# Performance work log

Hardware: AMD Instinct MI355X
Metric: run time of the kernel (lower is better)

The kernel has to match this reference:

```python
import jax, jax.numpy as jnp
import numpy as np

H = 16            # num_heads
NORM = 16.0       # gate normalizer
SCALE = 128.0 ** -0.5  # (embed_dim // num_heads) ** -0.5, per source
EPS = 1e-5


def setup_inputs() -> dict:
    key = jax.random.key(0)
    ks = jax.random.split(key, 10)
    B, L, D = 2, 2048, 2048
    g = lambda k, shape, s: jax.random.normal(k, shape, jnp.float32) * s
    return {
        "x": g(ks[0], (B, L, D), 1.0),
        "Wq": g(ks[1], (1024, D), 0.02),
        "Wk": g(ks[2], (1024, D), 0.02),
        "Wkg1": g(ks[3], (16, D), 0.02),
        "Wkg2": g(ks[4], (1024, 16), 0.05),
        "bkg2": jnp.zeros((1024,), jnp.float32),
        "Wv": g(ks[5], (D, D), 0.02),
        "Wg": g(ks[6], (D, D), 0.02),
        "bg": jnp.zeros((D,), jnp.float32),
        "Wo": g(ks[7], (D, D), 0.02),
    }


def _gla_core(x, Wq, Wk, Wkg1, Wkg2, bkg2, Wv, Wg, bg, Wo):
    B, L, D = x.shape
    q = x @ Wq.T                         # [B,L,1024]
    k = (x @ Wk.T) * SCALE               # [B,L,1024]
    kg = (x @ Wkg1.T) @ Wkg2.T + bkg2    # [B,L,1024] low-rank gate
    v = x @ Wv.T                         # [B,L,2048]
    gproj = x @ Wg.T + bg                # [B,L,2048]

    dk = q.shape[-1] // H   # 64
    dv = D // H             # 128
    heads = lambda t, dh: t.reshape(B, L, H, dh).transpose(0, 2, 1, 3)  # b h l d
    qh = heads(q, dk)
    kh = heads(k, dk)
    vh = heads(v, dv)
    gk = jax.nn.log_sigmoid(heads(kg, dk)) / NORM  # b h l dk

    # recurrence: S_t = diag(exp(gk_t)) S_{t-1} + k_t v_t^T ; o_t = q_t S_t
    tfirst = lambda t: t.transpose(2, 0, 1, 3)  # l b h d

    def step(S, inp):
        qt, kt, vt, gt = inp
        S = S * jnp.exp(gt)[..., None] + kt[..., None] * vt[..., None, :]
        ot = jnp.einsum('bhk,bhkv->bhv', qt, S)
        return S, ot

    S0 = jnp.zeros((B, H, dk, dv), x.dtype)
    _, os = jax.lax.scan(step, S0, (tfirst(qh), tfirst(kh), tfirst(vh), tfirst(gk)))
    o = os.transpose(1, 2, 0, 3)  # b h l dv

    # LayerNorm over head dim, no affine
    mu = o.mean(-1, keepdims=True)
    var = ((o - mu) ** 2).mean(-1, keepdims=True)
    o = (o - mu) * jax.lax.rsqrt(var + EPS)

    o = o.transpose(0, 2, 1, 3).reshape(B, L, D)  # b l (h dv)
    return (jax.nn.silu(gproj) * o) @ Wo.T


def reference(x, Wq, Wk, Wkg1, Wkg2, bkg2, Wv, Wg, bg, Wo):
    return _gla_core(x, Wq, Wk, Wkg1, Wkg2, bkg2, Wv, Wg, bg, Wo)
```

## Files before the change

### kernel.cpp

```cpp
#include <hip/hip_runtime.h>
#include <hip/hip_bf16.h>

using bf16x8 = __attribute__((ext_vector_type(8))) __bf16;
using fx4    = __attribute__((ext_vector_type(4))) float;
using us4    = __attribute__((ext_vector_type(4))) unsigned short;
using us8    = __attribute__((ext_vector_type(8))) unsigned short;

__device__ __forceinline__ float b2f(unsigned short u) {
    unsigned int x = ((unsigned int)u) << 16;
    return __builtin_bit_cast(float, x);
}
__device__ __forceinline__ unsigned short f2b(float f) {
    __hip_bfloat16 h = __float2bfloat16(f);
    return __builtin_bit_cast(unsigned short, h);
}
__device__ __forceinline__ float logsigmoidf(float z) {
    return fminf(z, 0.0f) - log1pf(expf(-fabsf(z)));
}

__device__ __forceinline__ void gl_lds16(const unsigned short* g, unsigned short* l) {
    __builtin_amdgcn_global_load_lds(
        (const __attribute__((address_space(1))) void*)g,
        (__attribute__((address_space(3))) void*)l, 16, 0, 0);
}

__device__ __forceinline__ bf16x8 frag64(const unsigned short* base, int row, int cq) {
    return *reinterpret_cast<const bf16x8*>(base + row * 64 + (((cq ^ (row & 7)) << 3)));
}
__device__ __forceinline__ int sw_idx(int row, int col) {
    return row * 64 + ((((col >> 3) ^ (row & 7)) << 3)) + (col & 7);
}

__global__ __launch_bounds__(256) void detect_kernel(
    const unsigned int* __restrict__ x, int* __restrict__ flag)
{
    __shared__ int bad[256];
    const int t = threadIdx.x;
    int b = 0;
#pragma unroll
    for (int i = 0; i < 16; ++i) {
        unsigned int w = x[t * 16 + i];
        float v = b2f((unsigned short)(w & 0xFFFFu));
        if (!(fabsf(v) < 1.0e6f)) b = 1;
    }
    bad[t] = b;
    __syncthreads();
    for (int s = 128; s > 0; s >>= 1) {
        if (t < s) bad[t] |= bad[t + s];
        __syncthreads();
    }
    if (t == 0) flag[0] = bad[0];
}

struct CvtArgs {
    const void* src[10];
    unsigned short* dst[10];
};

__global__ __launch_bounds__(256) void convert_all_kernel(
    CvtArgs a, const int* __restrict__ flag)
{
    const int pref[11] = {0, 8192, 10240, 12288, 12320, 12336, 12337,
                          16433, 20529, 20531, 24627};
    const int blk = blockIdx.x;
    int s = 0;
#pragma unroll
    for (int i = 1; i < 10; ++i) s += (blk >= pref[i]) ? 1 : 0;
    const int i0 = (blk - pref[s]) * 1024 + threadIdx.x * 4;
    if (*flag) {
        const float* sp = (const float*)a.src[s];
        fx4 v = *reinterpret_cast<const fx4*>(sp + i0);
        us4 r;
#pragma unroll
        for (int e = 0; e < 4; ++e) r[e] = f2b(v[e]);
        *reinterpret_cast<us4*>(a.dst[s] + i0) = r;
    } else {
        const unsigned short* sp = (const unsigned short*)a.src[s];
        *reinterpret_cast<us4*>(a.dst[s] + i0) =
            *reinterpret_cast<const us4*>(sp + i0);
    }
}

struct Seg3 {
    unsigned short* C0;
    unsigned short* C1;
    unsigned short* C2;
    const unsigned short* bias2;
};

__global__ __launch_bounds__(512, 2) void gemm_fused3_kernel(
    const unsigned short* __restrict__ A, const unsigned short* __restrict__ W,
    Seg3 segs, float scale_k)
{
    __shared__ __align__(16) unsigned short As[2 * 256 * 64];
    __shared__ __align__(16) unsigned short Bs[2 * 2 * 128 * 64];

    const int NT = 32, K = 2048;
    const int tid  = threadIdx.x;
    const int lane = tid & 63, wid = tid >> 6;
    const int quad = lane >> 4, l15 = lane & 15;
    const int wr = wid >> 2, wc = wid & 3;
    const int m0 = blockIdx.y * 256, n0 = blockIdx.x * 256;

    const unsigned short* Ab = A + (size_t)m0 * K;
    const unsigned short* Wb = W + (size_t)n0 * K;

    const int sx = ((tid & 7) ^ ((tid >> 3) & 7)) * 8;
    const unsigned short* pA[2][2];
    const unsigned short* pB[2][2];
#pragma unroll
    for (int mh = 0; mh < 2; ++mh)
#pragma unroll
        for (int j = 0; j < 2; ++j)
            pA[mh][j] = Ab + (size_t)(j * 128 + mh * 64 + (tid >> 3)) * K + sx;
#pragma unroll
    for (int nh = 0; nh < 2; ++nh)
#pragma unroll
        for (int j = 0; j < 2; ++j)
            pB[nh][j] = Wb + (size_t)((j * 2 + (tid >> 8)) * 64 + nh * 32 +
                                      ((tid >> 3) & 31)) * K + sx;

    fx4 acc[8][4];
#pragma unroll
    for (int i = 0; i < 8; ++i)
#pragma unroll
        for (int j = 0; j < 4; ++j) acc[i][j] = fx4{0.f, 0.f, 0.f, 0.f};

    auto stageA = [&](int mh, int tt) {
#pragma unroll
        for (int j = 0; j < 2; ++j)
            gl_lds16(pA[mh][j] + tt * 64,
                     As + (tt & 1) * 16384 + (j * 128 + mh * 64) * 64 + tid * 8);
    };
    auto stageB = [&](int nh, int tt) {
#pragma unroll
        for (int j = 0; j < 2; ++j)
            gl_lds16(pB[nh][j] + tt * 64,
                     Bs + (tt & 1) * 16384 + nh * 8192 + j * 4096 + tid * 8);
    };

    bf16x8 afr[4][2], bfr[2][2];
    const int x7 = l15 & 7;
    const int cswz0 = (quad ^ x7) << 3;
    const int cswz1 = ((quad + 4) ^ x7) << 3;
    int arow[4], brow[2];
#pragma unroll
    for (int mt = 0; mt < 4; ++mt) arow[mt] = (wr * 128 + mt * 16 + l15) * 64;
#pragma unroll
    for (int nt = 0; nt < 2; ++nt) brow[nt] = (wc * 32 + nt * 16 + l15) * 64;

    auto ldA = [&](int s, int mh) {
        const unsigned short* base = As + s * 16384 + mh * 4096;
#pragma unroll
        for (int mt = 0; mt < 4; ++mt) {
            afr[mt][0] = *(const bf16x8*)(base + arow[mt] + cswz0);
            afr[mt][1] = *(const bf16x8*)(base + arow[mt] + cswz1);
        }
    };
    auto ldB = [&](int s, int nh) {
        const unsigned short* base = Bs + s * 16384 + nh * 8192;
#pragma unroll
        for (int nt = 0; nt < 2; ++nt) {
            bfr[nt][0] = *(const bf16x8*)(base + brow[nt] + cswz0);
            bfr[nt][1] = *(const bf16x8*)(base + brow[nt] + cswz1);
        }
    };
    auto mma = [&](int mh, int nh) {
        __builtin_amdgcn_s_setprio(1);
#pragma unroll
        for (int mt = 0; mt < 4; ++mt)
#pragma unroll
            for (int nt = 0; nt < 2; ++nt) {
                acc[mh * 4 + mt][nh * 2 + nt] = __builtin_amdgcn_mfma_f32_16x16x32_bf16(
                    afr[mt][0], bfr[nt][0], acc[mh * 4 + mt][nh * 2 + nt], 0, 0, 0);
                acc[mh * 4 + mt][nh * 2 + nt] = __builtin_amdgcn_mfma_f32_16x16x32_bf16(
                    afr[mt][1], bfr[nt][1], acc[mh * 4 + mt][nh * 2 + nt], 0, 0, 0);
            }
        __builtin_amdgcn_s_setprio(0);
    };

    stageA(0, 0); stageB(0, 0); stageA(1, 0); stageB(1, 0);
    stageA(0, 1); stageB(0, 1);

    for (int t = 0; t < NT; ++t) {
        const int s = t & 1;
        if (t + 1 < NT) stageA(1, t + 1);
        if (t < NT - 1) asm volatile("s_waitcnt vmcnt(6)" ::: "memory");
        else            asm volatile("s_waitcnt vmcnt(0)" ::: "memory");
        asm volatile("s_barrier" ::: "memory");
        ldA(s, 0); ldB(s, 0);
        mma(0, 0);
        asm volatile("s_barrier" ::: "memory");
        if (t + 1 < NT) stageB(1, t + 1);
        ldB(s, 1);
        asm volatile("s_barrier" ::: "memory");
        mma(0, 1);
        asm volatile("s_barrier" ::: "memory");
        if (t + 2 < NT) stageA(0, t + 2);
        ldA(s, 1); ldB(s, 0);
        asm volatile("s_barrier" ::: "memory");
        mma(1, 0);
        asm volatile("s_barrier" ::: "memory");
        if (t + 2 < NT) stageB(0, t + 2);
        ldB(s, 1);
        asm volatile("s_barrier" ::: "memory");
        mma(1, 1);
        asm volatile("s_barrier" ::: "memory");
    }

    const int segi = n0 >> 11;
    unsigned short* Cs = (segi == 0) ? segs.C0 : ((segi == 1) ? segs.C1 : segs.C2);
#pragma unroll
    for (int j = 0; j < 4; ++j) {
        const int ncl = (n0 & 2047) + wc * 64 + j * 16 + l15;
        const float av = (segi == 0 && ncl >= 1024) ? scale_k : 1.0f;
        const float bv = (segi == 2) ? b2f(segs.bias2[ncl]) : 0.0f;
#pragma unroll
        for (int i = 0; i < 8; ++i) {
#pragma unroll
            for (int r = 0; r < 4; ++r) {
                const int mrow = m0 + wr * 128 + i * 16 + quad * 4 + r;
                float val = acc[i][j][r] * av + bv;
                if (segi == 2) val = val / (1.0f + __expf(-val));
                Cs[(size_t)mrow * 2048 + ncl] = f2b(val);
            }
        }
    }
}

__global__ __launch_bounds__(256) void gemm_bt_kernel(
    const unsigned short* __restrict__ A, const unsigned short* __restrict__ W,
    unsigned short* __restrict__ C, int M, int N, int K,
    const int* __restrict__ oflag)
{
    __shared__ __align__(16) unsigned short As[128 * 64];
    __shared__ __align__(16) unsigned short Bs[128 * 64];

    const int tid  = threadIdx.x;
    const int lane = tid & 63, wid = tid >> 6;
    const int quad = lane >> 4, l15 = lane & 15;
    const int wm = (wid & 1) * 64, wn = (wid >> 1) * 64;
    const int m0 = blockIdx.y * 128, n0 = blockIdx.x * 128;

    fx4 acc[4][4];
#pragma unroll
    for (int i = 0; i < 4; ++i)
#pragma unroll
        for (int j = 0; j < 4; ++j) acc[i][j] = fx4{0.f, 0.f, 0.f, 0.f};

    const int srow = lane >> 3;
    const int g8   = ((lane & 7) ^ srow) * 8;
    const int c8   = (lane & 7) * 8;
    const unsigned short* Ab = A + (size_t)m0 * K;
    const unsigned short* Wb = W + (size_t)n0 * K;

    for (int k0 = 0; k0 < K; k0 += 64) {
#pragma unroll
        for (int p = 0; p < 4; ++p) {
            const int la  = wid * 4 + p;
            const int row = la * 8 + srow;
            gl_lds16(Ab + (size_t)row * K + k0 + g8, As + row * 64 + c8);
            gl_lds16(Wb + (size_t)row * K + k0 + g8, Bs + row * 64 + c8);
        }
        __syncthreads();
#pragma unroll
        for (int ks = 0; ks < 2; ++ks) {
            const int cq = quad + ks * 4;
            bf16x8 af[4], bfr[4];
#pragma unroll
            for (int mt = 0; mt < 4; ++mt) af[mt] = frag64(As, wm + mt * 16 + l15, cq);
#pragma unroll
            for (int nt = 0; nt < 4; ++nt) bfr[nt] = frag64(Bs, wn + nt * 16 + l15, cq);
#pragma unroll
            for (int mt = 0; mt < 4; ++mt)
#pragma unroll
                for (int nt = 0; nt < 4; ++nt)
                    acc[mt][nt] = __builtin_amdgcn_mfma_f32_16x16x32_bf16(
                        af[mt], bfr[nt], acc[mt][nt], 0, 0, 0);
        }
        __syncthreads();
    }

    const int f32out = oflag ? *oflag : 0;
#pragma unroll
    for (int nt = 0; nt < 4; ++nt) {
        const int ncol = n0 + wn + nt * 16 + l15;
#pragma unroll
        for (int mt = 0; mt < 4; ++mt) {
#pragma unroll
            for (int r = 0; r < 4; ++r) {
                const int mrow = m0 + wm + mt * 16 + quad * 4 + r;
                float val = acc[mt][nt][r];
                const size_t idx = (size_t)mrow * N + ncol;
                if (f32out) ((float*)C)[idx] = val;
                else        C[idx] = f2b(val);
            }
        }
    }
}

__global__ __launch_bounds__(256) void gate1_kernel(
    const unsigned short* __restrict__ x, const unsigned short* __restrict__ Wkg1,
    const unsigned short* __restrict__ Wkg2, const unsigned short* __restrict__ bkg2,
    float* __restrict__ Ag)
{
    __shared__ float part[4][16];
    __shared__ float kgrow[16];
    const int m = blockIdx.x;
    const int tid = threadIdx.x;
    const int lane = tid & 63, w = tid >> 6;

    us8 xv = *reinterpret_cast<const us8*>(x + (size_t)m * 2048 + tid * 8);
    float xr[8];
#pragma unroll
    for (int e = 0; e < 8; ++e) xr[e] = b2f(xv[e]);

#pragma unroll
    for (int n = 0; n < 16; ++n) {
        us8 wv = *reinterpret_cast<const us8*>(Wkg1 + (size_t)n * 2048 + tid * 8);
        float s = 0.f;
#pragma unroll
        for (int e = 0; e < 8; ++e) s += xr[e] * b2f(wv[e]);
#pragma unroll
        for (int off = 1; off < 64; off <<= 1) s += __shfl_xor(s, off, 64);
        if (lane == 0) part[w][n] = s;
    }
    __syncthreads();
    if (tid < 16)
        kgrow[tid] = part[0][tid] + part[1][tid] + part[2][tid] + part[3][tid];
    __syncthreads();
    float kr[16];
#pragma unroll
    for (int j = 0; j < 16; ++j) kr[j] = kgrow[j];

    const int b = m >> 11, l = m & 2047;
    const int c0 = tid * 4;
    const int h = c0 >> 6, d0 = c0 & 63;
    fx4 gv;
#pragma unroll
    for (int qi = 0; qi < 4; ++qi) {
        const int c = c0 + qi;
        us8 w0 = *reinterpret_cast<const us8*>(Wkg2 + (size_t)c * 16);
        us8 w1 = *reinterpret_cast<const us8*>(Wkg2 + (size_t)c * 16 + 8);
        float z = b2f(bkg2[c]);
#pragma unroll
        for (int j = 0; j < 8; ++j) z += kr[j] * b2f(w0[j]) + kr[8 + j] * b2f(w1[j]);
        gv[qi] = logsigmoidf(z) * 0.0625f;
    }
    *reinterpret_cast<fx4*>(Ag + ((size_t)(b * 16 + h) * 2048 + l) * 64 + d0) = gv;
}

__global__ __launch_bounds__(256) void gate2_kernel(float* __restrict__ Ag)
{
    const int gidx = blockIdx.x * 256 + threadIdx.x;
    const int d = gidx & 63, ch = (gidx >> 6) & 31, bh = gidx >> 11;
    float* p = Ag + ((size_t)bh * 2048 + ch * 64) * 64 + d;
    float acc = 0.f;
#pragma unroll 8
    for (int t = 0; t < 64; ++t) {
        acc += p[(size_t)t * 64];
        p[(size_t)t * 64] = acc;
    }
}

__global__ __launch_bounds__(256) void pass1_kernel(
    const unsigned short* __restrict__ k, int kstr,
    const unsigned short* __restrict__ v,
    const float* __restrict__ Ag, float* __restrict__ Tc)
{
    __shared__ __align__(16) unsigned short kT[64 * 64];
    __shared__ __align__(16) unsigned short vT[128 * 64];

    const int blk = blockIdx.x;
    const int ch = blk & 31, bh = blk >> 5;
    const int b = bh >> 4, h = bh & 15;
    const int tid = threadIdx.x;
    const int lane = tid & 63, w = tid >> 6;
    const int quad = lane >> 4, l15 = lane & 15;

    const float* Abase = Ag + ((size_t)bh * 2048 + ch * 64) * 64;
    const unsigned short* kbase = k + ((size_t)(b * 2048 + ch * 64)) * kstr + h * 64;
    const unsigned short* vbase = v + ((size_t)(b * 2048 + ch * 64)) * 2048 + h * 128;

    {
        const int s = tid >> 2, d0 = (tid & 3) * 16;
        float av[16], a63[16];
        *(fx4*)(av)      = *(const fx4*)(Abase + (size_t)s * 64 + d0);
        *(fx4*)(av + 4)  = *(const fx4*)(Abase + (size_t)s * 64 + d0 + 4);
        *(fx4*)(av + 8)  = *(const fx4*)(Abase + (size_t)s * 64 + d0 + 8);
        *(fx4*)(av + 12) = *(const fx4*)(Abase + (size_t)s * 64 + d0 + 12);
        *(fx4*)(a63)      = *(const fx4*)(Abase + (size_t)63 * 64 + d0);
        *(fx4*)(a63 + 4)  = *(const fx4*)(Abase + (size_t)63 * 64 + d0 + 4);
        *(fx4*)(a63 + 8)  = *(const fx4*)(Abase + (size_t)63 * 64 + d0 + 8);
        *(fx4*)(a63 + 12) = *(const fx4*)(Abase + (size_t)63 * 64 + d0 + 12);
        us8 k0v = *(const us8*)(kbase + (size_t)s * kstr + d0);
        us8 k1v = *(const us8*)(kbase + (size_t)s * kstr + d0 + 8);
#pragma unroll
        for (int e = 0; e < 8; ++e) {
            kT[sw_idx(d0 + e, s)]     = f2b(b2f(k0v[e]) * __expf(a63[e] - av[e]));
            kT[sw_idx(d0 + 8 + e, s)] = f2b(b2f(k1v[e]) * __expf(a63[8 + e] - av[8 + e]));
        }
    }
    {
        const int s = tid >> 2, j0 = (tid & 3) * 32;
#pragma unroll
        for (int g2 = 0; g2 < 4; ++g2) {
            us8 vv = *(const us8*)(vbase + (size_t)s * 2048 + j0 + g2 * 8);
#pragma unroll
            for (int e = 0; e < 8; ++e) vT[sw_idx(j0 + g2 * 8 + e, s)] = vv[e];
        }
    }
    __syncthreads();

    bf16x8 bk[4][2];
#pragma unroll
    for (int nt = 0; nt < 4; ++nt) {
        bk[nt][0] = frag64(kT, nt * 16 + l15, quad);
        bk[nt][1] = frag64(kT, nt * 16 + l15, quad + 4);
    }
    fx4 acc[2][4];
#pragma unroll
    for (int mi = 0; mi < 2; ++mi)
#pragma unroll
        for (int nt = 0; nt < 4; ++nt) acc[mi][nt] = fx4{0.f, 0.f, 0.f, 0.f};
#pragma unroll
    for (int mi = 0; mi < 2; ++mi) {
        const int mrow = (w * 2 + mi) * 16 + l15;
        bf16x8 av0 = frag64(vT, mrow, quad);
        bf16x8 av1 = frag64(vT, mrow, quad + 4);
#pragma unroll
        for (int nt = 0; nt < 4; ++nt) {
            acc[mi][nt] = __builtin_amdgcn_mfma_f32_16x16x32_bf16(av0, bk[nt][0], acc[mi][nt], 0, 0, 0);
            acc[mi][nt] = __builtin_amdgcn_mfma_f32_16x16x32_bf16(av1, bk[nt][1], acc[mi][nt], 0, 0, 0);
        }
    }
    float* tb = Tc + (size_t)blk * 8192;
#pragma unroll
    for (int mi = 0; mi < 2; ++mi)
#pragma unroll
        for (int nt = 0; nt < 4; ++nt)
#pragma unroll
            for (int r = 0; r < 4; ++r) {
                const int j = (w * 2 + mi) * 16 + quad * 4 + r;
                const int d = nt * 16 + l15;
                tb[(size_t)j * 64 + d] = acc[mi][nt][r];
            }
}

__global__ __launch_bounds__(256) void combine_kernel(
    float* __restrict__ TS, const float* __restrict__ Ag)
{
    const int blk = blockIdx.x;
    const int js = blk & 7, bh = blk >> 3;
    const int tid = threadIdx.x;
    const int j = js * 16 + (tid >> 4), d0 = (tid & 15) * 4;
    fx4 S = fx4{0.f, 0.f, 0.f, 0.f};
    const float* Abase = Ag + (size_t)bh * 2048 * 64;
    for (int c = 0; c < 32; ++c) {
        float* p = TS + ((size_t)(bh * 32 + c)) * 8192 + (size_t)j * 64 + d0;
        fx4 t = *(const fx4*)p;
        *(fx4*)p = S;
        fx4 a = *(const fx4*)(Abase + ((size_t)c * 64 + 63) * 64 + d0);
#pragma unroll
        for (int e = 0; e < 4; ++e) S[e] = S[e] * __expf(a[e]) + t[e];
    }
}

__global__ __launch_bounds__(256) void pass2_kernel(
    const unsigned short* __restrict__ q, const unsigned short* __restrict__ k,
    int qkstr,
    const unsigned short* __restrict__ v, const float* __restrict__ Ag,
    const float* __restrict__ Sst, const unsigned short* __restrict__ sg,
    unsigned short* __restrict__ y)
{
    __shared__ __align__(16) unsigned short qs[64 * 64];
    __shared__ __align__(16) unsigned short ksh[64 * 64];
    __shared__ __align__(16) unsigned short vT[128 * 64];
    __shared__ __align__(16) unsigned short Pb[64 * 64];
    __shared__ __align__(16) unsigned short Ob[64 * 144];

    const int blk = blockIdx.x;
    const int ch = blk & 31, bh = blk >> 5;
    const int b = bh >> 4, h = bh & 15;
    const int tid = threadIdx.x;
    const int lane = tid & 63, w = tid >> 6;
    const int quad = lane >> 4, l15 = lane & 15;

    const float* Abase = Ag + ((size_t)bh * 2048 + ch * 64) * 64;
    const unsigned short* qbase = q + ((size_t)(b * 2048 + ch * 64)) * qkstr + h * 64;
    const unsigned short* kbase = k + ((size_t)(b * 2048 + ch * 64)) * qkstr + h * 64;
    const unsigned short* vbase = v + ((size_t)(b * 2048 + ch * 64)) * 2048 + h * 128;

    {
        const int t = tid >> 2, d0 = (tid & 3) * 16;
        float av[16];
        *(fx4*)(av)      = *(const fx4*)(Abase + (size_t)t * 64 + d0);
        *(fx4*)(av + 4)  = *(const fx4*)(Abase + (size_t)t * 64 + d0 + 4);
        *(fx4*)(av + 8)  = *(const fx4*)(Abase + (size_t)t * 64 + d0 + 8);
        *(fx4*)(av + 12) = *(const fx4*)(Abase + (size_t)t * 64 + d0 + 12);
        us8 q0 = *(const us8*)(qbase + (size_t)t * qkstr + d0);
        us8 q1 = *(const us8*)(qbase + (size_t)t * qkstr + d0 + 8);
        us8 k0 = *(const us8*)(kbase + (size_t)t * qkstr + d0);
        us8 k1 = *(const us8*)(kbase + (size_t)t * qkstr + d0 + 8);
        us8 qo0, qo1, ko0, ko1;
#pragma unroll
        for (int e = 0; e < 8; ++e) {
            float e0 = __expf(av[e]),     n0 = __expf(-av[e]);
            float e1 = __expf(av[8 + e]), n1 = __expf(-av[8 + e]);
            qo0[e] = f2b(b2f(q0[e]) * e0);
            qo1[e] = f2b(b2f(q1[e]) * e1);
            ko0[e] = f2b(b2f(k0[e]) * n0);
            ko1[e] = f2b(b2f(k1[e]) * n1);
        }
        const int c0 = d0 >> 3, t7 = t & 7;
        *(us8*)(qs  + t * 64 + ((c0 ^ t7) << 3))       = qo0;
        *(us8*)(qs  + t * 64 + (((c0 + 1) ^ t7) << 3)) = qo1;
        *(us8*)(ksh + t * 64 + ((c0 ^ t7) << 3))       = ko0;
        *(us8*)(ksh + t * 64 + (((c0 + 1) ^ t7) << 3)) = ko1;
    }
    {
        const int s = tid >> 2, j0 = (tid & 3) * 32;
#pragma unroll
        for (int g2 = 0; g2 < 4; ++g2) {
            us8 vv = *(const us8*)(vbase + (size_t)s * 2048 + j0 + g2 * 8);
#pragma unroll
            for (int e = 0; e < 8; ++e) vT[sw_idx(j0 + g2 * 8 + e, s)] = vv[e];
        }
    }
    __syncthreads();

    bf16x8 aQ0 = frag64(qs, w * 16 + l15, quad);
    bf16x8 aQ1 = frag64(qs, w * 16 + l15, quad + 4);
    fx4 accP[4];
#pragma unroll
    for (int nt = 0; nt < 4; ++nt) accP[nt] = fx4{0.f, 0.f, 0.f, 0.f};
#pragma unroll
    for (int nt = 0; nt < 4; ++nt) {
        bf16x8 bK0 = frag64(ksh, nt * 16 + l15, quad);
        bf16x8 bK1 = frag64(ksh, nt * 16 + l15, quad + 4);
        accP[nt] = __builtin_amdgcn_mfma_f32_16x16x32_bf16(aQ0, bK0, accP[nt], 0, 0, 0);
        accP[nt] = __builtin_amdgcn_mfma_f32_16x16x32_bf16(aQ1, bK1, accP[nt], 0, 0, 0);
    }
#pragma unroll
    for (int nt = 0; nt < 4; ++nt)
#pragma unroll
        for (int r = 0; r < 4; ++r) {
            const int t = w * 16 + quad * 4 + r;
            const int s = nt * 16 + l15;
            Pb[sw_idx(t, s)] = f2b((s <= t) ? accP[nt][r] : 0.0f);
        }
    __syncthreads();

    bf16x8 aP0 = frag64(Pb, w * 16 + l15, quad);
    bf16x8 aP1 = frag64(Pb, w * 16 + l15, quad + 4);
    const float* ST = Sst + (size_t)blk * 8192;
    fx4 accO[8];
#pragma unroll
    for (int nt = 0; nt < 8; ++nt) accO[nt] = fx4{0.f, 0.f, 0.f, 0.f};
#pragma unroll
    for (int nt = 0; nt < 8; ++nt) {
        const int j = nt * 16 + l15;
        bf16x8 bV0 = frag64(vT, j, quad);
        bf16x8 bV1 = frag64(vT, j, quad + 4);
        const float* sp = ST + (size_t)j * 64 + quad * 8;
        fx4 s0a = *(const fx4*)(sp),      s0b = *(const fx4*)(sp + 4);
        fx4 s1a = *(const fx4*)(sp + 32), s1b = *(const fx4*)(sp + 36);
        us8 hi0u, lo0u, hi1u, lo1u;
#pragma unroll
        for (int e = 0; e < 4; ++e) {
            unsigned short hh;
            hh = f2b(s0a[e]); hi0u[e] = hh;     lo0u[e]     = f2b(s0a[e] - b2f(hh));
            hh = f2b(s0b[e]); hi0u[4 + e] = hh; lo0u[4 + e] = f2b(s0b[e] - b2f(hh));
            hh = f2b(s1a[e]); hi1u[e] = hh;     lo1u[e]     = f2b(s1a[e] - b2f(hh));
            hh = f2b(s1b[e]); hi1u[4 + e] = hh; lo1u[4 + e] = f2b(s1b[e] - b2f(hh));
        }
        bf16x8 hi0 = __builtin_bit_cast(bf16x8, hi0u);
        bf16x8 lo0 = __builtin_bit_cast(bf16x8, lo0u);
        bf16x8 hi1 = __builtin_bit_cast(bf16x8, hi1u);
        bf16x8 lo1 = __builtin_bit_cast(bf16x8, lo1u);
        accO[nt] = __builtin_amdgcn_mfma_f32_16x16x32_bf16(aP0, bV0, accO[nt], 0, 0, 0);
        accO[nt] = __builtin_amdgcn_mfma_f32_16x16x32_bf16(aP1, bV1, accO[nt], 0, 0, 0);
        accO[nt] = __builtin_amdgcn_mfma_f32_16x16x32_bf16(aQ0, hi0, accO[nt], 0, 0, 0);
        accO[nt] = __builtin_amdgcn_mfma_f32_16x16x32_bf16(aQ1, hi1, accO[nt], 0, 0, 0);
        accO[nt] = __builtin_amdgcn_mfma_f32_16x16x32_bf16(aQ0, lo0, accO[nt], 0, 0, 0);
        accO[nt] = __builtin_amdgcn_mfma_f32_16x16x32_bf16(aQ1, lo1, accO[nt], 0, 0, 0);
    }

    float sum1[4] = {0.f, 0.f, 0.f, 0.f}, sum2[4] = {0.f, 0.f, 0.f, 0.f};
#pragma unroll
    for (int nt = 0; nt < 8; ++nt)
#pragma unroll
        for (int r = 0; r < 4; ++r) {
            float ov = accO[nt][r];
            sum1[r] += ov;
            sum2[r] += ov * ov;
        }
#pragma unroll
    for (int m = 1; m < 16; m <<= 1)
#pragma unroll
        for (int r = 0; r < 4; ++r) {
            sum1[r] += __shfl_xor(sum1[r], m, 64);
            sum2[r] += __shfl_xor(sum2[r], m, 64);
        }
    float mu[4], inv[4];
#pragma unroll
    for (int r = 0; r < 4; ++r) {
        mu[r] = sum1[r] * (1.0f / 128.0f);
        float var = sum2[r] * (1.0f / 128.0f) - mu[r] * mu[r];
        inv[r] = rsqrtf(var + 1e-5f);
    }
#pragma unroll
    for (int nt = 0; nt < 8; ++nt)
#pragma unroll
        for (int r = 0; r < 4; ++r) {
            const int t = w * 16 + quad * 4 + r;
            Ob[t * 144 + nt * 16 + l15] = f2b((accO[nt][r] - mu[r]) * inv[r]);
        }
    __syncthreads();

    {
        const int t2 = tid >> 2, jg = (tid & 3) * 32;
        const size_t obase = ((size_t)(b * 2048 + ch * 64 + t2)) * 2048 + h * 128 + jg;
#pragma unroll
        for (int g2 = 0; g2 < 4; ++g2) {
            us8 ob = *(const us8*)(Ob + t2 * 144 + jg + g2 * 8);
            us8 gv = *(const us8*)(sg + obase + g2 * 8);
            us8 ov;
#pragma unroll
            for (int e = 0; e < 8; ++e) ov[e] = f2b(b2f(gv[e]) * b2f(ob[e]));
            *(us8*)(y + obase + g2 * 8) = ov;
        }
    }
}

extern "C" void kernel_launch(void* const* d_in, const int* in_sizes, int n_in,
                              void* d_out, int out_size, void* d_ws, size_t ws_size,
                              hipStream_t stream)
{
    unsigned short* out = (unsigned short*)d_out;

    char* ws = (char*)d_ws;
    size_t off = 0;
    auto alloc = [&](size_t bytes) -> void* {
        void* p = ws + off;
        off += (bytes + 255) & ~(size_t)255;
        return p;
    };
    unsigned short* xb    = (unsigned short*)alloc((size_t)4096 * 2048 * 2);
    unsigned short* Wbig  = (unsigned short*)alloc((size_t)6144 * 2048 * 2);
    unsigned short* Wkg1b = (unsigned short*)alloc((size_t)16 * 2048 * 2);
    unsigned short* Wkg2b = (unsigned short*)alloc((size_t)1024 * 16 * 2);
    unsigned short* bkg2b = (unsigned short*)alloc((size_t)1024 * 2);
    unsigned short* bgb   = (unsigned short*)alloc((size_t)2048 * 2);
    unsigned short* Wob   = (unsigned short*)alloc((size_t)2048 * 2048 * 2);
    unsigned short* qkb  = (unsigned short*)alloc((size_t)4096 * 2048 * 2);
    unsigned short* vb   = (unsigned short*)alloc((size_t)4096 * 2048 * 2);
    unsigned short* sgb  = (unsigned short*)alloc((size_t)4096 * 2048 * 2);
    unsigned short* yb   = (unsigned short*)alloc((size_t)4096 * 2048 * 2);
    float*          Agb  = (float*)alloc((size_t)4096 * 1024 * 4);
    float*          TS   = (float*)alloc((size_t)1024 * 8192 * 4);
    int*            flag = (int*)alloc(256);

    detect_kernel<<<1, 256, 0, stream>>>((const unsigned int*)d_in[0], flag);

    CvtArgs ca;
    ca.src[0] = d_in[0]; ca.dst[0] = xb;
    ca.src[1] = d_in[1]; ca.dst[1] = Wbig;
    ca.src[2] = d_in[2]; ca.dst[2] = Wbig + (size_t)1024 * 2048;
    ca.src[3] = d_in[3]; ca.dst[3] = Wkg1b;
    ca.src[4] = d_in[4]; ca.dst[4] = Wkg2b;
    ca.src[5] = d_in[5]; ca.dst[5] = bkg2b;
    ca.src[6] = d_in[6]; ca.dst[6] = Wbig + (size_t)2048 * 2048;
    ca.src[7] = d_in[7]; ca.dst[7] = Wbig + (size_t)4096 * 2048;
    ca.src[8] = d_in[8]; ca.dst[8] = bgb;
    ca.src[9] = d_in[9]; ca.dst[9] = Wob;
    convert_all_kernel<<<24627, 256, 0, stream>>>(ca, flag);

    const float SCALE = 0.08838834764831845f;

    Seg3 segs;
    segs.C0 = qkb; segs.C1 = vb; segs.C2 = sgb; segs.bias2 = bgb;
    gemm_fused3_kernel<<<dim3(24, 16), 512, 0, stream>>>(xb, Wbig, segs, SCALE);

    gate1_kernel<<<4096, 256, 0, stream>>>(xb, Wkg1b, Wkg2b, bkg2b, Agb);
    gate2_kernel<<<256, 256, 0, stream>>>(Agb);
    pass1_kernel<<<1024, 256, 0, stream>>>(qkb + 1024, 2048, vb, Agb, TS);
    combine_kernel<<<256, 256, 0, stream>>>(TS, Agb);
    pass2_kernel<<<1024, 256, 0, stream>>>(qkb, qkb + 1024, 2048, vb, Agb, TS, sgb, yb);
    gemm_bt_kernel<<<dim3(16, 32), 256, 0, stream>>>(yb, Wob, out, 4096, 2048, 2048, flag);
}
```

Measured before the change: 459.0 us.

## Restructure GEMM pipeline waits, parallelize gate reduction, pre-split state into bf16 hi/lo

The big projection GEMM loop now issues LDS fragment loads before the next global-to-LDS stage, adds sched_barriers, and moves the vmcnt wait to the end of each iteration so global loads overlap more with MFMA work. The gate1 kernel replaces the per-wave shuffle reduction with an LDS partial-sum transpose and a shorter 16-lane shuffle. The combine kernel now writes chunk states already split into bf16 hi/lo pairs, so pass2 loads packed bf16 and shuffles instead of converting fp32 per fragment. This cuts conversion work and state traffic in pass2, but it relies on the new wait counts being correct for the changed load order.

Result: faster. 418.9 us (-8.7%).

```diff
diff --git a/kernel.cpp b/kernel.cpp
--- a/kernel.cpp
+++ b/kernel.cpp
@@ -181,30 +181,36 @@
 
     stageA(0, 0); stageB(0, 0); stageA(1, 0); stageB(1, 0);
     stageA(0, 1); stageB(0, 1);
+    asm volatile("s_waitcnt vmcnt(4)" ::: "memory");
+    asm volatile("s_barrier" ::: "memory");
 
     for (int t = 0; t < NT; ++t) {
         const int s = t & 1;
+        ldA(s, 0); ldB(s, 0);
         if (t + 1 < NT) stageA(1, t + 1);
-        if (t < NT - 1) asm volatile("s_waitcnt vmcnt(6)" ::: "memory");
-        else            asm volatile("s_waitcnt vmcnt(0)" ::: "memory");
         asm volatile("s_barrier" ::: "memory");
-        ldA(s, 0); ldB(s, 0);
+        __builtin_amdgcn_sched_barrier(0);
         mma(0, 0);
         asm volatile("s_barrier" ::: "memory");
+        ldB(s, 1);
         if (t + 1 < NT) stageB(1, t + 1);
-        ldB(s, 1);
         asm volatile("s_barrier" ::: "memory");
+        __builtin_amdgcn_sched_barrier(0);
         mma(0, 1);
         asm volatile("s_barrier" ::: "memory");
+        ldA(s, 1); ldB(s, 0);
         if (t + 2 < NT) stageA(0, t + 2);
-        ldA(s, 1); ldB(s, 0);
         asm volatile("s_barrier" ::: "memory");
+        __builtin_amdgcn_sched_barrier(0);
         mma(1, 0);
         asm volatile("s_barrier" ::: "memory");
+        ldB(s, 1);
         if (t + 2 < NT) stageB(0, t + 2);
-        ldB(s, 1);
         asm volatile("s_barrier" ::: "memory");
+        __builtin_amdgcn_sched_barrier(0);
         mma(1, 1);
+        if (t < NT - 2)       asm volatile("s_waitcnt vmcnt(4)" ::: "memory");
+        else if (t == NT - 2) asm volatile("s_waitcnt vmcnt(0)" ::: "memory");
         asm volatile("s_barrier" ::: "memory");
     }
 
@@ -304,11 +310,10 @@
     const unsigned short* __restrict__ Wkg2, const unsigned short* __restrict__ bkg2,
     float* __restrict__ Ag)
 {
-    __shared__ float part[4][16];
+    __shared__ float part[16][257];
     __shared__ float kgrow[16];
     const int m = blockIdx.x;
     const int tid = threadIdx.x;
-    const int lane = tid & 63, w = tid >> 6;
 
     us8 xv = *reinterpret_cast<const us8*>(x + (size_t)m * 2048 + tid * 8);
     float xr[8];
@@ -321,13 +326,18 @@
         float s = 0.f;
 #pragma unroll
         for (int e = 0; e < 8; ++e) s += xr[e] * b2f(wv[e]);
-#pragma unroll
-        for (int off = 1; off < 64; off <<= 1) s += __shfl_xor(s, off, 64);
-        if (lane == 0) part[w][n] = s;
+        part[n][tid] = s;
     }
     __syncthreads();
-    if (tid < 16)
-        kgrow[tid] = part[0][tid] + part[1][tid] + part[2][tid] + part[3][tid];
+    {
+        const int n = tid >> 4, i = tid & 15;
+        float s = 0.f;
+#pragma unroll
+        for (int k2 = 0; k2 < 16; ++k2) s += part[n][i + k2 * 16];
+#pragma unroll
+        for (int off = 1; off < 16; off <<= 1) s += __shfl_xor(s, off, 64);
+        if (i == 0) kgrow[n] = s;
+    }
     __syncthreads();
     float kr[16];
 #pragma unroll
@@ -459,7 +469,13 @@
     for (int c = 0; c < 32; ++c) {
         float* p = TS + ((size_t)(bh * 32 + c)) * 8192 + (size_t)j * 64 + d0;
         fx4 t = *(const fx4*)p;
-        *(fx4*)p = S;
+        us8 pk;
+#pragma unroll
+        for (int e = 0; e < 4; ++e) {
+            pk[e]     = f2b(S[e]);
+            pk[4 + e] = f2b(S[e] - b2f(pk[e]));
+        }
+        *(us8*)p = pk;
         fx4 a = *(const fx4*)(Abase + ((size_t)c * 64 + 63) * 64 + d0);
 #pragma unroll
         for (int e = 0; e < 4; ++e) S[e] = S[e] * __expf(a[e]) + t[e];
@@ -553,7 +569,7 @@
 
     bf16x8 aP0 = frag64(Pb, w * 16 + l15, quad);
     bf16x8 aP1 = frag64(Pb, w * 16 + l15, quad + 4);
-    const float* ST = Sst + (size_t)blk * 8192;
+    const unsigned short* SP = (const unsigned short*)(Sst + (size_t)blk * 8192);
     fx4 accO[8];
 #pragma unroll
     for (int nt = 0; nt < 8; ++nt) accO[nt] = fx4{0.f, 0.f, 0.f, 0.f};
@@ -562,18 +578,15 @@
         const int j = nt * 16 + l15;
         bf16x8 bV0 = frag64(vT, j, quad);
         bf16x8 bV1 = frag64(vT, j, quad + 4);
-        const float* sp = ST + (size_t)j * 64 + quad * 8;
-        fx4 s0a = *(const fx4*)(sp),      s0b = *(const fx4*)(sp + 4);
-        fx4 s1a = *(const fx4*)(sp + 32), s1b = *(const fx4*)(sp + 36);
-        us8 hi0u, lo0u, hi1u, lo1u;
-#pragma unroll
-        for (int e = 0; e < 4; ++e) {
-            unsigned short hh;
-            hh = f2b(s0a[e]); hi0u[e] = hh;     lo0u[e]     = f2b(s0a[e] - b2f(hh));
-            hh = f2b(s0b[e]); hi0u[4 + e] = hh; lo0u[4 + e] = f2b(s0b[e] - b2f(hh));
-            hh = f2b(s1a[e]); hi1u[e] = hh;     lo1u[e]     = f2b(s1a[e] - b2f(hh));
-            hh = f2b(s1b[e]); hi1u[4 + e] = hh; lo1u[4 + e] = f2b(s1b[e] - b2f(hh));
-        }
+        const unsigned short* sb = SP + (size_t)(j * 64 + quad * 8) * 2;
+        us8 ga = *(const us8*)(sb);
+        us8 gb = *(const us8*)(sb + 8);
+        us8 gc = *(const us8*)(sb + 64);
+        us8 gd = *(const us8*)(sb + 72);
+        us8 hi0u = __builtin_shufflevector(ga, gb, 0, 1, 2, 3, 8, 9, 10, 11);
+        us8 lo0u = __builtin_shufflevector(ga, gb, 4, 5, 6, 7, 12, 13, 14, 15);
+        us8 hi1u = __builtin_shufflevector(gc, gd, 0, 1, 2, 3, 8, 9, 10, 11);
+        us8 lo1u = __builtin_shufflevector(gc, gd, 4, 5, 6, 7, 12, 13, 14, 15);
         bf16x8 hi0 = __builtin_bit_cast(bf16x8, hi0u);
         bf16x8 lo0 = __builtin_bit_cast(bf16x8, lo0u);
         bf16x8 hi1 = __builtin_bit_cast(bf16x8, hi1u);
```
